# Optimization experiments

Measured on AMD Instinct MI355X. Metric: run time of the kernel, lower is better.

## Reference

```python
import jax, jax.numpy as jnp
import numpy as np

# Module constants (match init_kwargs / torch defaults)
NUM_HEADS = 8
A, B_COEF, C_COEF = 0.5, 1.0, 1.0
EPS = 1e-12  # torch F.normalize eps


def _l2_normalize(x):
    n = jnp.maximum(jnp.linalg.norm(x, axis=-1, keepdims=True), EPS)
    return x / n


def setup_inputs() -> dict:
    key = jax.random.key(0)
    ks = jax.random.split(key, 4)
    Bb, N, C = 1, 4096, 384
    x = jax.random.normal(ks[0], (Bb, N, C), dtype=jnp.float32)
    qkv_w = jax.random.normal(ks[1], (3 * C, C), dtype=jnp.float32) * 0.02
    qkv_b = jnp.zeros((3 * C,), dtype=jnp.float32)
    proj_w = jax.random.normal(ks[2], (C, C), dtype=jnp.float32) * 0.02
    proj_b = jnp.zeros((C,), dtype=jnp.float32)
    temperature = jnp.ones((1, NUM_HEADS, 1, 1), dtype=jnp.float32)
    return {"x": x, "qkv_w": qkv_w, "qkv_b": qkv_b, "proj_w": proj_w,
            "proj_b": proj_b, "temperature": temperature}


def reference(x, qkv_w, qkv_b, proj_w, proj_b, temperature):
    Bb, N, C = x.shape
    H = NUM_HEADS
    d = C // H
    scale = d ** 0.25

    qkv = x @ qkv_w.T + qkv_b                       # (B, N, 3C)
    qkv = qkv.reshape(Bb, N, 3, H, d).transpose(2, 0, 3, 1, 4)  # (3, B, H, N, d)
    q, k, v = qkv[0], qkv[1], qkv[2]
    q = q * (C ** -0.5)

    # efficient attention (N > N0 = d^2 + d + 1)
    v1 = jnp.concatenate([jnp.ones((Bb, H, N, 1), dtype=v.dtype), v], axis=-1)  # (B,H,N,d+1)
    # normalize_input=True path
    q = _l2_normalize(q) * (scale * temperature)
    k = _l2_normalize(k) * scale
    v1 = v1 / N

    # kv_mod = box(k,k)^T @ v1  ->  (B, H, d, d, d+1)
    kv_mod = jnp.einsum('bhni,bhnj,bhnf->bhijf', k, k, v1)
    # quadratic term: a * box(q,q) @ kv_mod
    y = A * jnp.einsum('bhni,bhnj,bhijf->bhnf', q, q, kv_mod)
    # linear term: scale^2 * b * q @ (k^T @ v1)
    kv = jnp.einsum('bhnd,bhnf->bhdf', k, v1)
    y = y + (scale ** 2) * B_COEF * jnp.einsum('bhnd,bhdf->bhnf', q, kv)
    # constant term: scale^4 * c * sum_n v1
    y = y + (scale ** 4) * C_COEF * jnp.sum(v1, axis=-2, keepdims=True)

    y_norm, y_out = y[..., :1], y[..., 1:]
    out = y_out / y_norm                             # (B, H, N, d)

    out = out.transpose(0, 2, 1, 3).reshape(Bb, N, C)
    out = out @ proj_w.T + proj_b
    return out
```

## Files before the change

### kernel.cpp

```cpp
#include <hip/hip_runtime.h>

#define HN 8
#define NN 4096
#define CC 384
#define DD 48
#define DP 64
#define NPAIR 1225
#define PPAD 1280
#define MPF 52

typedef unsigned short ushort;
typedef unsigned int uint;
typedef __attribute__((ext_vector_type(8))) short short8;
typedef __attribute__((ext_vector_type(4))) float f32x4;

__device__ __forceinline__ float4 ld4(const float* p){ return *reinterpret_cast<const float4*>(p); }
__device__ __forceinline__ void st4(float* p, const float4& v){ *reinterpret_cast<float4*>(p) = v; }

__device__ __forceinline__ uint bf16rtn(float x){
  uint u = __float_as_uint(x);
  return (u + 0x7FFFu + ((u >> 16) & 1u)) >> 16;
}

__global__ __launch_bounds__(256) void split_f32(const float* __restrict__ in,
                                                 ushort* __restrict__ hi,
                                                 ushort* __restrict__ lo,
                                                 int n4) {
  int idx = blockIdx.x * 256 + threadIdx.x;
  if (idx >= n4) return;
  float4 v = ld4(in + (size_t)idx * 4);
  float bv[4] = {v.x, v.y, v.z, v.w};
  uint hu[2], lu[2];
#pragma unroll
  for (int e = 0; e < 2; ++e) {
    float x0 = bv[2*e], x1 = bv[2*e+1];
    uint h0 = bf16rtn(x0), h1 = bf16rtn(x1);
    float d0 = x0 - __uint_as_float(h0 << 16);
    float d1 = x1 - __uint_as_float(h1 << 16);
    hu[e] = h0 | (h1 << 16);
    lu[e] = (__float_as_uint(d0) >> 16) | (__float_as_uint(d1) & 0xFFFF0000u);
  }
  *reinterpret_cast<uint2*>(hi + (size_t)idx*4) = make_uint2(hu[0], hu[1]);
  *reinterpret_cast<uint2*>(lo + (size_t)idx*4) = make_uint2(lu[0], lu[1]);
}

#define GST 40
__global__ __launch_bounds__(256) void gemm_bf16(const ushort* __restrict__ Ah,
                                                 const ushort* __restrict__ Al,
                                                 const float*  __restrict__ Bw,
                                                 const float*  __restrict__ bias,
                                                 float* __restrict__ Cm,
                                                 int M, int Nc, int K) {
  __shared__ ushort AsH[2][128*GST], AsL[2][128*GST];
  __shared__ ushort BsH[2][64*GST],  BsL[2][64*GST];
  const int tid = threadIdx.x;
  const int n0 = blockIdx.x * 64;
  const int m0 = blockIdx.y * 128;
  const int lane = tid & 63, wv = tid >> 6;
  const int wr = wv >> 1, wc = wv & 1;
  const int lr = lane & 15, lg = lane >> 4;
  const int ar = tid >> 1, ap = (tid & 1) << 4;
  const int br = tid >> 2, bp = (tid & 3) << 3;
  const ushort* gAh = Ah + (size_t)(m0 + ar) * K + ap;
  const ushort* gAl = Al + (size_t)(m0 + ar) * K + ap;
  const float*  gB  = Bw + (size_t)(n0 + br) * K + bp;
  uint4 rah0, rah1, ral0, ral1;
  float4 rb0, rb1;
#define G_LOAD(T) { int kk = (T)*32; \
    rah0 = *reinterpret_cast<const uint4*>(gAh + kk); \
    rah1 = *reinterpret_cast<const uint4*>(gAh + kk + 8); \
    ral0 = *reinterpret_cast<const uint4*>(gAl + kk); \
    ral1 = *reinterpret_cast<const uint4*>(gAl + kk + 8); \
    rb0 = ld4(gB + kk); rb1 = ld4(gB + kk + 4); }
#define G_WRITE(BUF) { \
    *reinterpret_cast<uint4*>(&AsH[BUF][ar*GST+ap])   = rah0; \
    *reinterpret_cast<uint4*>(&AsH[BUF][ar*GST+ap+8]) = rah1; \
    *reinterpret_cast<uint4*>(&AsL[BUF][ar*GST+ap])   = ral0; \
    *reinterpret_cast<uint4*>(&AsL[BUF][ar*GST+ap+8]) = ral1; \
    float bv[8] = {rb0.x,rb0.y,rb0.z,rb0.w,rb1.x,rb1.y,rb1.z,rb1.w}; \
    uint hu[4], lu[4]; \
    _Pragma("unroll") for (int e = 0; e < 4; ++e) { \
      float x0 = bv[2*e], x1 = bv[2*e+1]; \
      uint h0 = bf16rtn(x0), h1 = bf16rtn(x1); \
      float d0 = x0 - __uint_as_float(h0 << 16); \
      float d1 = x1 - __uint_as_float(h1 << 16); \
      hu[e] = h0 | (h1 << 16); \
      lu[e] = (__float_as_uint(d0) >> 16) | (__float_as_uint(d1) & 0xFFFF0000u); } \
    *reinterpret_cast<uint4*>(&BsH[BUF][br*GST+bp]) = make_uint4(hu[0],hu[1],hu[2],hu[3]); \
    *reinterpret_cast<uint4*>(&BsL[BUF][br*GST+bp]) = make_uint4(lu[0],lu[1],lu[2],lu[3]); }

  f32x4 acc[4][2];
#pragma unroll
  for (int pf = 0; pf < 4; ++pf)
#pragma unroll
    for (int ff = 0; ff < 2; ++ff) acc[pf][ff] = (f32x4)0.f;

  G_LOAD(0);
  G_WRITE(0);
  G_LOAD(1);
  const int NT = K / 32;
  int cur = 0;
  __syncthreads();
  for (int t = 0; t < NT; ++t) {
    short8 a_h[4], a_l[4], b_h[2], b_l[2];
#pragma unroll
    for (int pf = 0; pf < 4; ++pf) {
      int row = wr*64 + pf*16 + lr;
      a_h[pf] = *reinterpret_cast<const short8*>(&AsH[cur][row*GST + lg*8]);
      a_l[pf] = *reinterpret_cast<const short8*>(&AsL[cur][row*GST + lg*8]);
    }
#pragma unroll
    for (int ff = 0; ff < 2; ++ff) {
      int col = wc*32 + ff*16 + lr;
      b_h[ff] = *reinterpret_cast<const short8*>(&BsH[cur][col*GST + lg*8]);
      b_l[ff] = *reinterpret_cast<const short8*>(&BsL[cur][col*GST + lg*8]);
    }
    if (t < NT-1) { G_WRITE(cur^1); }
    if (t < NT-2) { G_LOAD(t+2); }
#pragma unroll
    for (int pf = 0; pf < 4; ++pf)
#pragma unroll
      for (int ff = 0; ff < 2; ++ff) {
        acc[pf][ff] = __builtin_amdgcn_mfma_f32_16x16x32_bf16(a_h[pf], b_h[ff], acc[pf][ff], 0, 0, 0);
        acc[pf][ff] = __builtin_amdgcn_mfma_f32_16x16x32_bf16(a_h[pf], b_l[ff], acc[pf][ff], 0, 0, 0);
        acc[pf][ff] = __builtin_amdgcn_mfma_f32_16x16x32_bf16(a_l[pf], b_h[ff], acc[pf][ff], 0, 0, 0);
      }
    __syncthreads();
    cur ^= 1;
  }
#pragma unroll
  for (int pf = 0; pf < 4; ++pf)
#pragma unroll
    for (int ff = 0; ff < 2; ++ff) {
      int col = n0 + wc*32 + ff*16 + lr;
      float bs = bias[col];
#pragma unroll
      for (int reg = 0; reg < 4; ++reg) {
        int row = m0 + wr*64 + pf*16 + lg*4 + reg;
        Cm[(size_t)row*Nc + col] = acc[pf][ff][reg] + bs;
      }
    }
#undef G_LOAD
#undef G_WRITE
}

__global__ __launch_bounds__(256) void prep2(const float* __restrict__ qkv,
                                             const float* __restrict__ temperature,
                                             float* __restrict__ Qb,
                                             float* __restrict__ KbT,
                                             ushort* __restrict__ VhT,
                                             ushort* __restrict__ VlT) {
  __shared__ float Ks[64*65];
  __shared__ float Vs[64*65];
  const int nb = blockIdx.x;
  const int h  = blockIdx.y;
  const int lane = threadIdx.x & 63;
  const int w = threadIdx.x >> 6;
  const float temp = temperature[h];
  const float CINV = 0.05103103630798288f;
  const float S4   = 2.6321480259049848f;
  for (int r = 0; r < 16; ++r) {
    const int nl = w*16 + r;
    const int n  = nb*64 + nl;
    const float* row = qkv + (size_t)n * (3*CC) + h * DD;
    float qv = (lane < DD) ? row[lane] : 0.f;
    float kv = (lane < DD) ? row[CC + lane] : 0.f;
    float vv = (lane >= 1 && lane <= DD) ? row[2*CC + lane - 1] : 0.f;
    float qs = qv * CINV;
    float q2 = qs * qs;
    float k2 = kv * kv;
#pragma unroll
    for (int off = 32; off > 0; off >>= 1) {
      q2 += __shfl_xor(q2, off);
      k2 += __shfl_xor(k2, off);
    }
    float qn = qs / fmaxf(sqrtf(q2), 1e-12f) * (S4 * temp);
    float kn = kv / fmaxf(sqrtf(k2), 1e-12f) * S4;
    float qo = (lane < DD) ? qn : ((lane == DD) ? 6.928203230275509f : 0.f);
    float ko = (lane < DD) ? kn : ((lane == DD) ? 1.f : 0.f);
    float vo = (lane == 0) ? (1.f/NN) : ((lane <= DD) ? vv * (1.f/NN) : 0.f);
    Qb[((size_t)h * NN + n) * DP + lane] = qo;
    Ks[nl*65 + lane] = ko;
    Vs[nl*65 + lane] = vo;
  }
  __syncthreads();
  const int ch = threadIdx.x >> 2;
  const int q4 = threadIdx.x & 3;
  float kc[16], vc[16];
#pragma unroll
  for (int e = 0; e < 16; ++e) {
    int nl = q4*16 + e;
    kc[e] = Ks[nl*65 + ch];
    vc[e] = Vs[nl*65 + ch];
  }
  size_t tbase = ((size_t)h*64 + ch) * NN + nb*64 + q4*16;
#pragma unroll
  for (int e = 0; e < 16; e += 4)
    st4(KbT + tbase + e, make_float4(kc[e], kc[e+1], kc[e+2], kc[e+3]));
  uint hu[8], lu[8];
#pragma unroll
  for (int e = 0; e < 8; ++e) {
    float v0 = vc[2*e], v1 = vc[2*e+1];
    uint h0 = bf16rtn(v0), h1 = bf16rtn(v1);
    float d0 = v0 - __uint_as_float(h0 << 16);
    float d1 = v1 - __uint_as_float(h1 << 16);
    uint t0 = __float_as_uint(d0), t1 = __float_as_uint(d1);
    hu[e] = h0 | (h1 << 16);
    lu[e] = (t0 >> 16) | (t1 & 0xFFFF0000u);
  }
  *reinterpret_cast<uint4*>(VhT + tbase)     = make_uint4(hu[0],hu[1],hu[2],hu[3]);
  *reinterpret_cast<uint4*>(VhT + tbase + 8) = make_uint4(hu[4],hu[5],hu[6],hu[7]);
  *reinterpret_cast<uint4*>(VlT + tbase)     = make_uint4(lu[0],lu[1],lu[2],lu[3]);
  *reinterpret_cast<uint4*>(VlT + tbase + 8) = make_uint4(lu[4],lu[5],lu[6],lu[7]);
}

#define KST 40
#define KNST 36
__global__ __launch_bounds__(256) void kvmod_mfma(const float* __restrict__ KbT,
                                                  const ushort* __restrict__ VhT,
                                                  const ushort* __restrict__ VlT,
                                                  float* __restrict__ Mp) {
  __shared__ ushort KKh[256*KST];
  __shared__ ushort KKl[256*KST];
  __shared__ float  KnS[64*KNST];
  __shared__ ushort VhS[64*KST];
  __shared__ ushort VlS[64*KST];
  const int tid  = threadIdx.x;
  const int p0   = blockIdx.x * 256;
  const int h    = blockIdx.y;
  const int part = blockIdx.z;
  const int nbase = part * 512;
  int ii = 63, jj = 63;
  {
    int pg = p0 + tid;
    if (pg < NPAIR) {
      int i = 0, rem = pg;
      while (rem >= 49 - i) { rem -= 49 - i; ++i; }
      ii = i; jj = i + rem;
    }
  }
  const float* krow_i = &KnS[ii*KNST];
  const float* krow_j = &KnS[jj*KNST];
  const int sch = tid >> 2;
  const int sq  = tid & 3;
  const size_t kgbase = ((size_t)h*64 + sch) * NN + nbase;
  const int lane = tid & 63, wv = tid >> 6;
  const int lr = lane & 15, lg = lane >> 4;
  f32x4 acc[4][4];
#pragma unroll
  for (int a = 0; a < 4; ++a)
#pragma unroll
    for (int b = 0; b < 4; ++b) acc[a][b] = (f32x4)0.f;

  for (int t = 0; t < 16; ++t) {
    const int k0 = t * 32;
    __syncthreads();
    {
      float4 a0 = ld4(KbT + kgbase + k0 + sq*8);
      float4 a1 = ld4(KbT + kgbase + k0 + sq*8 + 4);
      st4(&KnS[sch*KNST + sq*8], a0);
      st4(&KnS[sch*KNST + sq*8 + 4], a1);
      *reinterpret_cast<uint4*>(&VhS[sch*KST + sq*8]) =
          *reinterpret_cast<const uint4*>(VhT + kgbase + k0 + sq*8);
      *reinterpret_cast<uint4*>(&VlS[sch*KST + sq*8]) =
          *reinterpret_cast<const uint4*>(VlT + kgbase + k0 + sq*8);
    }
    __syncthreads();
    {
      uint hu[16], lu[16];
#pragma unroll
      for (int g = 0; g < 8; ++g) {
        float4 a = ld4(krow_i + g*4);
        float4 b = ld4(krow_j + g*4);
        float m0 = a.x*b.x, m1 = a.y*b.y, m2 = a.z*b.z, m3 = a.w*b.w;
        uint h0 = bf16rtn(m0), h1 = bf16rtn(m1), h2 = bf16rtn(m2), h3 = bf16rtn(m3);
        float d0 = m0 - __uint_as_float(h0 << 16);
        float d1 = m1 - __uint_as_float(h1 << 16);
        float d2 = m2 - __uint_as_float(h2 << 16);
        float d3 = m3 - __uint_as_float(h3 << 16);
        uint t0 = __float_as_uint(d0), t1 = __float_as_uint(d1);
        uint t2 = __float_as_uint(d2), t3 = __float_as_uint(d3);
        hu[2*g]   = h0 | (h1 << 16);
        hu[2*g+1] = h2 | (h3 << 16);
        lu[2*g]   = (t0 >> 16) | (t1 & 0xFFFF0000u);
        lu[2*g+1] = (t2 >> 16) | (t3 & 0xFFFF0000u);
      }
      uint4* dh = reinterpret_cast<uint4*>(&KKh[tid*KST]);
      uint4* dl = reinterpret_cast<uint4*>(&KKl[tid*KST]);
      dh[0] = make_uint4(hu[0],hu[1],hu[2],hu[3]);
      dh[1] = make_uint4(hu[4],hu[5],hu[6],hu[7]);
      dh[2] = make_uint4(hu[8],hu[9],hu[10],hu[11]);
      dh[3] = make_uint4(hu[12],hu[13],hu[14],hu[15]);
      dl[0] = make_uint4(lu[0],lu[1],lu[2],lu[3]);
      dl[1] = make_uint4(lu[4],lu[5],lu[6],lu[7]);
      dl[2] = make_uint4(lu[8],lu[9],lu[10],lu[11]);
      dl[3] = make_uint4(lu[12],lu[13],lu[14],lu[15]);
    }
    __syncthreads();
    short8 ah[4], al[4], bh[4], bl[4];
#pragma unroll
    for (int pf = 0; pf < 4; ++pf) {
      int prow = wv*64 + pf*16 + lr;
      ah[pf] = *reinterpret_cast<const short8*>(&KKh[prow*KST + lg*8]);
      al[pf] = *reinterpret_cast<const short8*>(&KKl[prow*KST + lg*8]);
    }
#pragma unroll
    for (int ff = 0; ff < 4; ++ff) {
      int frow = ff*16 + lr;
      bh[ff] = *reinterpret_cast<const short8*>(&VhS[frow*KST + lg*8]);
      bl[ff] = *reinterpret_cast<const short8*>(&VlS[frow*KST + lg*8]);
    }
#pragma unroll
    for (int pf = 0; pf < 4; ++pf)
#pragma unroll
      for (int ff = 0; ff < 4; ++ff) {
        acc[pf][ff] = __builtin_amdgcn_mfma_f32_16x16x32_bf16(ah[pf], bh[ff], acc[pf][ff], 0, 0, 0);
        acc[pf][ff] = __builtin_amdgcn_mfma_f32_16x16x32_bf16(ah[pf], bl[ff], acc[pf][ff], 0, 0, 0);
        acc[pf][ff] = __builtin_amdgcn_mfma_f32_16x16x32_bf16(al[pf], bh[ff], acc[pf][ff], 0, 0, 0);
      }
  }
  float* out = Mp + ((size_t)(part*HN + h) * PPAD + p0 + wv*64) * MPF;
#pragma unroll
  for (int pf = 0; pf < 4; ++pf)
#pragma unroll
    for (int ff = 0; ff < 4; ++ff) {
      int f = ff*16 + lr;
      if (f < MPF) {
#pragma unroll
        for (int reg = 0; reg < 4; ++reg) {
          int prow = pf*16 + lg*4 + reg;
          out[prow*MPF + f] = acc[pf][ff][reg];
        }
      }
    }
}

__global__ __launch_bounds__(256) void reduce_mirror(const float* __restrict__ Mp,
                                                     ushort* __restrict__ Mbh,
                                                     ushort* __restrict__ Mbl,
                                                     float* __restrict__ Mnorm) {
  const int pb = blockIdx.x;
  const int h  = blockIdx.y;
  const int pl = threadIdx.x & 63;
  const int fq0 = threadIdx.x >> 6;
  const int p = pb*64 + pl;
  if (p >= NPAIR) return;
  int i = 0, rem = p;
  while (rem >= 49 - i) { rem -= 49 - i; ++i; }
  const int j = i + rem;
  for (int fq = fq0; fq < 13; fq += 4) {
    float4 s = make_float4(0.f, 0.f, 0.f, 0.f);
#pragma unroll
    for (int part = 0; part < 8; ++part) {
      float4 a = ld4(Mp + ((size_t)(part*HN + h) * PPAD + p) * MPF + fq*4);
      s.x += a.x; s.y += a.y; s.z += a.z; s.w += a.w;
    }
    float sv[4] = {s.x, s.y, s.z, s.w};
#pragma unroll
    for (int c = 0; c < 4; ++c) {
      int f = fq*4 + c;
      float v = sv[c];
      uint hb = bf16rtn(v);
      float d = v - __uint_as_float(hb << 16);
      ushort lb = (ushort)(__float_as_uint(d) >> 16);
      size_t a1 = (((size_t)h*49 + i)*64 + f)*64 + j;
      size_t a2 = (((size_t)h*49 + j)*64 + f)*64 + i;
      Mbh[a1] = (ushort)hb; Mbl[a1] = lb;
      Mbh[a2] = (ushort)hb; Mbl[a2] = lb;
    }
    if (p == NPAIR-1) st4(&Mnorm[h*64 + fq*4], s);
  }
}

__global__ __launch_bounds__(256, 3) void y_mfma(const float* __restrict__ Qb,
                                                 const ushort* __restrict__ Mbh,
                                                 const ushort* __restrict__ Mbl,
                                                 float* __restrict__ Yp) {
  __shared__ float QT[28*128];
  __shared__ ushort Mt[2][2][32*64];
  const int tid = threadIdx.x;
  const int h = blockIdx.y;
  const int n0 = blockIdx.x * 128;
  const int zi = blockIdx.z >> 1;
  const int zf = blockIdx.z & 1;
  const int ibase = zi * 25;
  const int ni = zi ? 24 : 25;
  const int lane = tid & 63;
  const int wv = tid >> 6;
  const int lr = lane & 15, lg = lane >> 4;

  {
    const int ng = (ni + 3) >> 2;
    for (int v = tid; v < ng*128; v += 256) {
      int r = v & 127;
      int cg = v >> 7;
      float4 q = ld4(Qb + ((size_t)h*NN + n0 + r)*DP + ibase + cg*4);
      QT[(cg*4+0)*128 + r] = q.x;
      QT[(cg*4+1)*128 + r] = q.y;
      QT[(cg*4+2)*128 + r] = q.z;
      QT[(cg*4+3)*128 + r] = q.w;
    }
  }
  short8 ah[2][2], al[2][2];
#pragma unroll
  for (int m = 0; m < 2; ++m) {
    const float* qr = Qb + ((size_t)h*NN + n0 + wv*32 + m*16 + lr)*DP + lg*8;
#pragma unroll
    for (int kc = 0; kc < 2; ++kc) {
      float4 v0 = ld4(qr + kc*32);
      float4 v1 = ld4(qr + kc*32 + 4);
      float qv[8] = {v0.x,v0.y,v0.z,v0.w,v1.x,v1.y,v1.z,v1.w};
      union { uint u[4]; short8 s; } chh, cll;
#pragma unroll
      for (int e = 0; e < 4; ++e) {
        float x0 = qv[2*e], x1 = qv[2*e+1];
        uint h0 = bf16rtn(x0), h1 = bf16rtn(x1);
        float d0 = x0 - __uint_as_float(h0 << 16);
        float d1 = x1 - __uint_as_float(h1 << 16);
        chh.u[e] = h0 | (h1 << 16);
        cll.u[e] = (__float_as_uint(d0) >> 16) | (__float_as_uint(d1) & 0xFFFF0000u);
      }
      ah[m][kc] = chh.s;
      al[m][kc] = cll.s;
    }
  }
  const int sp   = tid >> 7;
  const int ss   = tid & 127;
  const int srow = ss >> 2;
  const int sc2  = (ss & 3) * 2;
  const ushort* gsrc = (sp ? Mbl : Mbh) + (size_t)h*49*4096 + (zf*32 + srow)*64 + sc2*8;
  uint4 pre[2];
#define Y_LOAD(I) { const uint4* gp = reinterpret_cast<const uint4*>(gsrc + (size_t)(I)*4096); \
    pre[0] = gp[0]; pre[1] = gp[1]; }
#define Y_WRITE(BUF) { _Pragma("unroll") for (int e = 0; e < 2; ++e) { \
    int slot = (sc2 + e) ^ (srow & 7); \
    *reinterpret_cast<uint4*>(&Mt[BUF][sp][srow*64 + slot*8]) = pre[e]; } }

  Y_LOAD(ibase);
  Y_WRITE(0);
  Y_LOAD(ibase+1);

  f32x4 ya[2][2];
#pragma unroll
  for (int m = 0; m < 2; ++m)
#pragma unroll
    for (int ff = 0; ff < 2; ++ff) ya[m][ff] = (f32x4)0.f;

  int cur = 0;
  __syncthreads();
  for (int li = 0; li < ni; ++li) {
    short8 bh[2][2], bl[2][2];
#pragma unroll
    for (int kc = 0; kc < 2; ++kc)
#pragma unroll
      for (int ff = 0; ff < 2; ++ff) {
        int row = ff*16 + lr;
        int slot = (kc*4 + lg) ^ (row & 7);
        bh[kc][ff] = *reinterpret_cast<const short8*>(&Mt[cur][0][row*64 + slot*8]);
        bl[kc][ff] = *reinterpret_cast<const short8*>(&Mt[cur][1][row*64 + slot*8]);
      }
    if (li < ni-1) { Y_WRITE(cur^1); }
    if (li < ni-2) { Y_LOAD(ibase+li+2); }
#pragma unroll
    for (int m = 0; m < 2; ++m) {
      float4 qi = ld4(&QT[li*128 + wv*32 + m*16 + lg*4]);
#pragma unroll
      for (int ff = 0; ff < 2; ++ff) {
        f32x4 acc = (f32x4)0.f;
        acc = __builtin_amdgcn_mfma_f32_16x16x32_bf16(ah[m][0], bh[0][ff], acc, 0, 0, 0);
        acc = __builtin_amdgcn_mfma_f32_16x16x32_bf16(ah[m][0], bl[0][ff], acc, 0, 0, 0);
        acc = __builtin_amdgcn_mfma_f32_16x16x32_bf16(al[m][0], bh[0][ff], acc, 0, 0, 0);
        acc = __builtin_amdgcn_mfma_f32_16x16x32_bf16(ah[m][1], bh[1][ff], acc, 0, 0, 0);
        acc = __builtin_amdgcn_mfma_f32_16x16x32_bf16(ah[m][1], bl[1][ff], acc, 0, 0, 0);
        acc = __builtin_amdgcn_mfma_f32_16x16x32_bf16(al[m][1], bh[1][ff], acc, 0, 0, 0);
        ya[m][ff][0] += qi.x * acc[0];
        ya[m][ff][1] += qi.y * acc[1];
        ya[m][ff][2] += qi.z * acc[2];
        ya[m][ff][3] += qi.w * acc[3];
      }
    }
    __syncthreads();
    cur ^= 1;
  }
  float* out = Yp + ((size_t)(zi*HN + h) * NN) * 64;
#pragma unroll
  for (int m = 0; m < 2; ++m)
#pragma unroll
    for (int ff = 0; ff < 2; ++ff) {
      int f = zf*32 + ff*16 + lr;
#pragma unroll
      for (int reg = 0; reg < 4; ++reg) {
        int row = n0 + wv*32 + m*16 + lg*4 + reg;
        out[(size_t)row*64 + f] = ya[m][ff][reg];
      }
    }
#undef Y_LOAD
#undef Y_WRITE
}

__global__ __launch_bounds__(256) void y_combine(const float* __restrict__ Yp,
                                                 const float* __restrict__ Mnorm,
                                                 ushort* __restrict__ AttnH,
                                                 ushort* __restrict__ AttnL) {
  const int h = blockIdx.y;
  const int t = threadIdx.x;
  const int r = blockIdx.x*64 + (t >> 2);
  const int fq = t & 3;
  const int lane = t & 63;
  const float* p0 = Yp + ((size_t)h*NN + r)*64 + fq*16;
  const float* p1 = Yp + ((size_t)(HN+h)*NN + r)*64 + fq*16;
  float y[16];
#pragma unroll
  for (int g = 0; g < 4; ++g) {
    float4 a = ld4(p0 + g*4);
    float4 b = ld4(p1 + g*4);
    float4 m = ld4(Mnorm + h*64 + fq*16 + g*4);
    y[g*4+0] = 0.5f*(a.x+b.x) + 24.f*m.x;
    y[g*4+1] = 0.5f*(a.y+b.y) + 24.f*m.y;
    y[g*4+2] = 0.5f*(a.z+b.z) + 24.f*m.z;
    y[g*4+3] = 0.5f*(a.w+b.w) + 24.f*m.w;
  }
  float y0 = __shfl(y[0], lane & ~3);
  float inv = 1.f / y0;
#pragma unroll
  for (int e = 0; e < 16; ++e) {
    int f = fq*16 + e;
    if (f >= 1 && f <= DD) {
      float o = y[e] * inv;
      uint hb = bf16rtn(o);
      float d = o - __uint_as_float(hb << 16);
      size_t a = (size_t)r*CC + h*DD + (f-1);
      AttnH[a] = (ushort)hb;
      AttnL[a] = (ushort)(__float_as_uint(d) >> 16);
    }
  }
}

extern "C" void kernel_launch(void* const* d_in, const int* in_sizes, int n_in,
                              void* d_out, int out_size, void* d_ws, size_t ws_size,
                              hipStream_t stream) {
  const float* x      = (const float*)d_in[0];
  const float* qkv_w  = (const float*)d_in[1];
  const float* qkv_b  = (const float*)d_in[2];
  const float* proj_w = (const float*)d_in[3];
  const float* proj_b = (const float*)d_in[4];
  const float* temp   = (const float*)d_in[5];
  float* ws = (float*)d_ws;

  float*  qkv  = ws;
  float*  Mp   = ws;
  float*  Yp   = ws;
  float*  Qb   = ws + 4718592;
  ushort* Xh   = (ushort*)(ws + 6815744);
  ushort* Xl   = Xh + 1572864;
  float*  KbT  = ws + 6815744;
  ushort* Mbh  = (ushort*)(ws + 6815744);
  ushort* Mbl  = Mbh + 1605632;
  float*  Mnorm= ws + 6815744 + 1605632;
  ushort* VhT  = (ushort*)(ws + 8912896);
  ushort* VlT  = (ushort*)(ws + 9961472);
  ushort* AttnH= (ushort*)(ws + 8912896);
  ushort* AttnL= AttnH + 1572864;

  split_f32<<<1536, 256, 0, stream>>>(x, Xh, Xl, NN*CC/4);
  {
    dim3 g(1152/64, 4096/128);
    gemm_bf16<<<g, 256, 0, stream>>>(Xh, Xl, qkv_w, qkv_b, qkv, 4096, 1152, 384);
  }
  {
    dim3 g(64, HN);
    prep2<<<g, 256, 0, stream>>>(qkv, temp, Qb, KbT, VhT, VlT);
  }
  {
    dim3 g(PPAD/256, HN, 8);
    kvmod_mfma<<<g, 256, 0, stream>>>(KbT, VhT, VlT, Mp);
  }
  hipMemsetAsync((void*)Mbh, 0, 2*(size_t)1605632*2 + 2048, stream);
  {
    dim3 g(PPAD/64, HN);
    reduce_mirror<<<g, 256, 0, stream>>>(Mp, Mbh, Mbl, Mnorm);
  }
  {
    dim3 g(4096/128, HN, 4);
    y_mfma<<<g, 256, 0, stream>>>(Qb, Mbh, Mbl, Yp);
  }
  {
    dim3 g(4096/64, HN);
    y_combine<<<g, 256, 0, stream>>>(Yp, Mnorm, AttnH, AttnL);
  }
  {
    dim3 g(384/64, 4096/128);
    gemm_bf16<<<g, 256, 0, stream>>>(AttnH, AttnL, proj_w, proj_b, (float*)d_out, 4096, 384, 384);
  }
}
```

Before: 202.9 us.

## Load M fragments directly from global into registers, drop LDS staging

The y_mfma kernel used to stage the M hi/lo tiles cooperatively into a double-buffered shared-memory tile and then read MFMA operands from LDS, with a __syncthreads every iteration. Now each lane loads its bf16 B-fragments straight from global memory into registers, with a two-stage register double buffer and a manually unrolled loop. This removes the LDS traffic and the per-iteration barriers. In exchange it raises register pressure and relies on L2/cache hits, since the four waves redundantly fetch the same M data.

After: 239.1 us. +17.8%, slower.

```diff
diff --git a/kernel.cpp b/kernel.cpp
--- a/kernel.cpp
+++ b/kernel.cpp
@@ -377,7 +377,6 @@
                                                  const ushort* __restrict__ Mbl,
                                                  float* __restrict__ Yp) {
   __shared__ float QT[28*128];
-  __shared__ ushort Mt[2][2][32*64];
   const int tid = threadIdx.x;
   const int h = blockIdx.y;
   const int n0 = blockIdx.x * 128;
@@ -424,21 +423,29 @@
       al[m][kc] = cll.s;
     }
   }
-  const int sp   = tid >> 7;
-  const int ss   = tid & 127;
-  const int srow = ss >> 2;
-  const int sc2  = (ss & 3) * 2;
-  const ushort* gsrc = (sp ? Mbl : Mbh) + (size_t)h*49*4096 + (zf*32 + srow)*64 + sc2*8;
-  uint4 pre[2];
-#define Y_LOAD(I) { const uint4* gp = reinterpret_cast<const uint4*>(gsrc + (size_t)(I)*4096); \
-    pre[0] = gp[0]; pre[1] = gp[1]; }
-#define Y_WRITE(BUF) { _Pragma("unroll") for (int e = 0; e < 2; ++e) { \
-    int slot = (sc2 + e) ^ (srow & 7); \
-    *reinterpret_cast<uint4*>(&Mt[BUF][sp][srow*64 + slot*8]) = pre[e]; } }
-
-  Y_LOAD(ibase);
-  Y_WRITE(0);
-  Y_LOAD(ibase+1);
+  const ushort* gH = Mbh + (((size_t)h*49 + ibase)*64 + zf*32)*64 + lr*64 + lg*8;
+  const ushort* gL = Mbl + (((size_t)h*49 + ibase)*64 + zf*32)*64 + lr*64 + lg*8;
+#define RC(p) (*reinterpret_cast<const short8*>(p))
+#define LOADF(BH, BL, LI) { size_t sb = (size_t)(LI)*4096; \
+    BH[0][0] = RC(gH + sb);               BH[0][1] = RC(gH + sb + 1024); \
+    BH[1][0] = RC(gH + sb + 32);          BH[1][1] = RC(gH + sb + 1024 + 32); \
+    BL[0][0] = RC(gL + sb);               BL[0][1] = RC(gL + sb + 1024); \
+    BL[1][0] = RC(gL + sb + 32);          BL[1][1] = RC(gL + sb + 1024 + 32); }
+#define COMPUTE(BH, BL, LI) { \
+    _Pragma("unroll") for (int m = 0; m < 2; ++m) { \
+      float4 qi = ld4(&QT[(LI)*128 + wv*32 + m*16 + lg*4]); \
+      _Pragma("unroll") for (int ff = 0; ff < 2; ++ff) { \
+        f32x4 acc = (f32x4)0.f; \
+        acc = __builtin_amdgcn_mfma_f32_16x16x32_bf16(ah[m][0], BH[0][ff], acc, 0, 0, 0); \
+        acc = __builtin_amdgcn_mfma_f32_16x16x32_bf16(ah[m][0], BL[0][ff], acc, 0, 0, 0); \
+        acc = __builtin_amdgcn_mfma_f32_16x16x32_bf16(al[m][0], BH[0][ff], acc, 0, 0, 0); \
+        acc = __builtin_amdgcn_mfma_f32_16x16x32_bf16(ah[m][1], BH[1][ff], acc, 0, 0, 0); \
+        acc = __builtin_amdgcn_mfma_f32_16x16x32_bf16(ah[m][1], BL[1][ff], acc, 0, 0, 0); \
+        acc = __builtin_amdgcn_mfma_f32_16x16x32_bf16(al[m][1], BH[1][ff], acc, 0, 0, 0); \
+        ya[m][ff][0] += qi.x * acc[0]; \
+        ya[m][ff][1] += qi.y * acc[1]; \
+        ya[m][ff][2] += qi.z * acc[2]; \
+        ya[m][ff][3] += qi.w * acc[3]; } } }
 
   f32x4 ya[2][2];
 #pragma unroll
@@ -446,42 +453,20 @@
 #pragma unroll
     for (int ff = 0; ff < 2; ++ff) ya[m][ff] = (f32x4)0.f;
 
-  int cur = 0;
+  short8 pAh[2][2], pAl[2][2];
+  short8 pBh[2][2], pBl[2][2];
+  LOADF(pAh, pAl, 0);
   __syncthreads();
-  for (int li = 0; li < ni; ++li) {
-    short8 bh[2][2], bl[2][2];
-#pragma unroll
-    for (int kc = 0; kc < 2; ++kc)
-#pragma unroll
-      for (int ff = 0; ff < 2; ++ff) {
-        int row = ff*16 + lr;
-        int slot = (kc*4 + lg) ^ (row & 7);
-        bh[kc][ff] = *reinterpret_cast<const short8*>(&Mt[cur][0][row*64 + slot*8]);
-        bl[kc][ff] = *reinterpret_cast<const short8*>(&Mt[cur][1][row*64 + slot*8]);
-      }
-    if (li < ni-1) { Y_WRITE(cur^1); }
-    if (li < ni-2) { Y_LOAD(ibase+li+2); }
-#pragma unroll
-    for (int m = 0; m < 2; ++m) {
-      float4 qi = ld4(&QT[li*128 + wv*32 + m*16 + lg*4]);
-#pragma unroll
-      for (int ff = 0; ff < 2; ++ff) {
-        f32x4 acc = (f32x4)0.f;
-        acc = __builtin_amdgcn_mfma_f32_16x16x32_bf16(ah[m][0], bh[0][ff], acc, 0, 0, 0);
-        acc = __builtin_amdgcn_mfma_f32_16x16x32_bf16(ah[m][0], bl[0][ff], acc, 0, 0, 0);
-        acc = __builtin_amdgcn_mfma_f32_16x16x32_bf16(al[m][0], bh[0][ff], acc, 0, 0, 0);
-        acc = __builtin_amdgcn_mfma_f32_16x16x32_bf16(ah[m][1], bh[1][ff], acc, 0, 0, 0);
-        acc = __builtin_amdgcn_mfma_f32_16x16x32_bf16(ah[m][1], bl[1][ff], acc, 0, 0, 0);
-        acc = __builtin_amdgcn_mfma_f32_16x16x32_bf16(al[m][1], bh[1][ff], acc, 0, 0, 0);
-        ya[m][ff][0] += qi.x * acc[0];
-        ya[m][ff][1] += qi.y * acc[1];
-        ya[m][ff][2] += qi.z * acc[2];
-        ya[m][ff][3] += qi.w * acc[3];
-      }
-    }
-    __syncthreads();
-    cur ^= 1;
-  }
+  int li = 0;
+  while (li + 1 < ni) {
+    LOADF(pBh, pBl, li+1);
+    COMPUTE(pAh, pAl, li);
+    if (li + 2 < ni) { LOADF(pAh, pAl, li+2); }
+    COMPUTE(pBh, pBl, li+1);
+    li += 2;
+  }
+  if (li < ni) { COMPUTE(pAh, pAl, li); }
+
   float* out = Yp + ((size_t)(zi*HN + h) * NN) * 64;
 #pragma unroll
   for (int m = 0; m < 2; ++m)
@@ -494,8 +479,9 @@
         out[(size_t)row*64 + f] = ya[m][ff][reg];
       }
     }
-#undef Y_LOAD
-#undef Y_WRITE
+#undef RC
+#undef LOADF
+#undef COMPUTE
 }
 
 __global__ __launch_bounds__(256) void y_combine(const float* __restrict__ Yp,
```
